# Kernel tuning notes

Hardware: AMD Instinct MI355X
Metric: run time of the kernel (lower is better)

The kernel has to match this reference:

```python
import jax, jax.numpy as jnp
import numpy as np

B, T_FRAMES, C, WS = 8, 8, 32, 128
N = 1024            # sample_size^2 points per frame
HW = WS * WS        # 16384 grid cells
BT = B * T_FRAMES


def setup_inputs() -> dict:
    key = jax.random.key(0)
    k1, k2, k3 = jax.random.split(key, 3)
    rng = np.random.default_rng(0)
    # per-frame grid-cell id for each of N points
    pose = rng.integers(0, HW, size=(BT, N))
    sorted_indices = np.argsort(pose, axis=1).astype(np.int32)
    sorted_pose = np.take_along_axis(pose, sorted_indices, axis=1)
    seq_unique_list = np.zeros((BT, N), dtype=np.int32)
    seq_unique_counts = np.zeros((BT, N), dtype=np.int32)
    for i in range(BT):
        u, c = np.unique(sorted_pose[i], return_counts=True)
        seq_unique_list[i, : len(u)] = u
        seq_unique_counts[i, : len(u)] = c
    return {
        "w_part": jax.random.normal(k1, (BT, N, C), dtype=jnp.float32),
        "sorted_indices": jnp.asarray(sorted_indices),
        "seq_unique_list": jnp.asarray(seq_unique_list),
        "seq_unique_counts": jnp.asarray(seq_unique_counts),
        "past_w": jax.random.normal(k2, (B, C, WS, WS), dtype=jnp.float32),
        "past_w_num_mask": jax.random.uniform(k3, (B, 1, WS, WS), dtype=jnp.float32) * 4.0,
        "T": T_FRAMES,
    }


def reference(w_part, sorted_indices, seq_unique_list, seq_unique_counts, past_w, past_w_num_mask, T):
    bt, n, c = w_part.shape
    b = bt // T
    ws = past_w.shape[2]
    hw = ws * ws
    # F.normalize(dim=-1), eps=1e-12
    wp = w_part / jnp.maximum(jnp.linalg.norm(w_part, axis=-1, keepdims=True), 1e-12)
    # gather: reorder points so same-cell points are contiguous
    gathered = jnp.take_along_axis(wp, sorted_indices[..., None].astype(jnp.int32), axis=1)  # (bt, n, c)
    counts = seq_unique_counts  # (bt, n) padded with zeros
    # segment id of each point from cumulative counts (points are sorted by cell)
    cum = jnp.cumsum(counts, axis=1)
    pt = jnp.arange(n)
    seg = jax.vmap(lambda cu: jnp.searchsorted(cu, pt, side='right'))(cum)  # (bt, n)
    sums = jax.vmap(lambda g, s: jax.ops.segment_sum(g, s, num_segments=n))(gathered, seg)  # (bt, n, c)
    means = sums / jnp.maximum(counts, 1)[..., None].astype(wp.dtype)
    # scatter means into dense grid; padded (count==0) slots routed out-of-bounds and dropped
    idx = jnp.where(counts > 0, seq_unique_list, hw)
    scat = jax.vmap(lambda m, i: jnp.zeros((hw, c), wp.dtype).at[i].set(m, mode='drop'))(means, idx)  # (bt, hw, c)
    mask = jax.vmap(lambda ct, i: jnp.zeros((hw,), wp.dtype).at[i].set(ct.astype(wp.dtype), mode='drop'))(counts, idx)
    new_w = scat.reshape(b, T, hw, c).mean(axis=1)                 # (b, hw, c)
    new_w = new_w.transpose(0, 2, 1).reshape(b, c, ws, ws)          # (b, c, ws, ws)
    w_num_mask = mask.reshape(b, T, hw).sum(axis=1).reshape(b, 1, ws, ws)
    # merge with past map; denominator is detached in the original
    new_w_num_mask = jax.lax.stop_gradient(w_num_mask) + jax.lax.stop_gradient(past_w_num_mask)
    new_w_num_mask = jnp.where(new_w_num_mask == 0, 1.0, new_w_num_mask)
    w = (new_w * w_num_mask + past_w * past_w_num_mask) / new_w_num_mask
    return w, new_w_num_mask
```

## Files before the change

kernel.cpp:

```cpp
#include <hip/hip_runtime.h>
#include <climits>

#define BATCH   8
#define TFRAMES 8
#define BT      (BATCH * TFRAMES)
#define NPTS    1024
#define NCH     32
#define WS      128
#define HW      (WS * WS)
#define CELLS   128
#define CHUNKS  (HW / CELLS)
#define CPAD    33
#define TPB     512

__global__ __launch_bounds__(256) void scan_kernel(
    const int* __restrict__ uniq_cnt,
    const int* __restrict__ uniq_list,
    int4*      __restrict__ entries,
    int*       __restrict__ ranges)
{
    __shared__ int s_key[NPTS];
    __shared__ int s_wsum[4];

    const int tid  = threadIdx.x;
    const int bt   = blockIdx.x;
    const int wave = tid >> 6;
    const int lane = tid & 63;

    const int4 c4 = reinterpret_cast<const int4*>(uniq_cnt + bt * NPTS)[tid];
    const int4 l4 = reinterpret_cast<const int4*>(uniq_list + bt * NPTS)[tid];
    s_key[tid * 4 + 0] = (c4.x > 0) ? l4.x : INT_MAX;
    s_key[tid * 4 + 1] = (c4.y > 0) ? l4.y : INT_MAX;
    s_key[tid * 4 + 2] = (c4.z > 0) ? l4.z : INT_MAX;
    s_key[tid * 4 + 3] = (c4.w > 0) ? l4.w : INT_MAX;

    const int lsum = c4.x + c4.y + c4.z + c4.w;

    int inc = lsum;
#pragma unroll
    for (int d = 1; d < 64; d <<= 1) {
        const int v = __shfl_up(inc, d);
        if (lane >= d) inc += v;
    }
    if (lane == 63) s_wsum[wave] = inc;
    __syncthreads();

    int woff = 0;
#pragma unroll
    for (int w = 0; w < 4; ++w)
        if (w < wave) woff += s_wsum[w];

    int st = woff + inc - lsum;
    int4* ep = entries + (size_t)bt * NPTS + tid * 4;
    ep[0] = make_int4(l4.x, c4.x, st, 0);             st += c4.x;
    ep[1] = make_int4(l4.y, c4.y, st, 0);             st += c4.y;
    ep[2] = make_int4(l4.z, c4.z, st, 0);             st += c4.z;
    ep[3] = make_int4(l4.w, c4.w, st, 0);

    if (tid <= CHUNKS) {
        const int X = tid * CELLS;
        int lo = 0, hi = NPTS;
        while (lo < hi) {
            const int mid = (lo + hi) >> 1;
            if (s_key[mid] < X) lo = mid + 1; else hi = mid;
        }
        ranges[bt * (CHUNKS + 1) + tid] = lo;
    }
}

__global__ __launch_bounds__(TPB) void tile_kernel(
    const float* __restrict__ w_part,
    const int*   __restrict__ sorted_idx,
    const int4*  __restrict__ entries,
    const int*   __restrict__ ranges,
    const float* __restrict__ past_w,
    const float* __restrict__ past_mask,
    float*       __restrict__ out_w,
    float*       __restrict__ out_mask)
{
    __shared__ float s_acc[CELLS][CPAD];
    __shared__ float s_mask[CELLS];

    const int tid      = threadIdx.x;
    const int b        = blockIdx.x / CHUNKS;
    const int chunk    = blockIdx.x % CHUNKS;
    const int cellBase = chunk * CELLS;

    const int cellq = tid & 31;
    const int cgrp  = tid >> 5;
    const int c0    = cgrp * 2;
    const int gc    = cellBase + cellq * 4;
    const size_t mbase = (size_t)b * HW + gc;
    const float4 pm4 = *reinterpret_cast<const float4*>(past_mask + mbase);
    const size_t a0 = ((size_t)b * NCH + c0) * HW + gc;
    const float4 pw0 = *reinterpret_cast<const float4*>(past_w + a0);
    const float4 pw1 = *reinterpret_cast<const float4*>(past_w + a0 + HW);

    float* flat = &s_acc[0][0];
    for (int i = tid; i < CELLS * CPAD; i += TPB) flat[i] = 0.0f;
    if (tid < CELLS) s_mask[tid] = 0.0f;
    __syncthreads();

    const int wave  = tid >> 6;
    const int lane  = tid & 63;
    const int slot  = lane >> 3;
    const int lane8 = lane & 7;

    const int bt = b * TFRAMES + wave;
    const int lo = ranges[bt * (CHUNKS + 1) + chunk];
    const int hi = ranges[bt * (CHUNKS + 1) + chunk + 1];
    const int4* __restrict__ ent = entries + (size_t)bt * NPTS;
    const int*  __restrict__ si  = sorted_idx + bt * NPTS;
    const float* __restrict__ wp = w_part + (size_t)bt * NPTS * NCH;

    for (int e0 = lo; e0 < hi; e0 += 8) {
        const int e = e0 + slot;
        if (e < hi) {
            const int4 meta = ent[e];
            const int cell  = meta.x;
            const int cnt   = meta.y;
            const int start = meta.z;
            float4 lacc = make_float4(0.f, 0.f, 0.f, 0.f);
            for (int p = start; p < start + cnt; ++p) {
                const int j = si[p];
                const float4 v = *reinterpret_cast<const float4*>(
                    wp + (size_t)j * NCH + lane8 * 4);
                float ss = v.x * v.x + v.y * v.y + v.z * v.z + v.w * v.w;
                ss += __shfl_xor(ss, 1);
                ss += __shfl_xor(ss, 2);
                ss += __shfl_xor(ss, 4);
                const float scale = 1.0f / fmaxf(sqrtf(ss), 1e-12f);
                lacc.x += v.x * scale;
                lacc.y += v.y * scale;
                lacc.z += v.z * scale;
                lacc.w += v.w * scale;
            }
            const float invc = 1.0f / (float)cnt;
            const int cl = cell - cellBase;
            float* ap = &s_acc[cl][lane8 * 4];
            atomicAdd(ap + 0, lacc.x * invc);
            atomicAdd(ap + 1, lacc.y * invc);
            atomicAdd(ap + 2, lacc.z * invc);
            atomicAdd(ap + 3, lacc.w * invc);
            if (lane8 == 0) atomicAdd(&s_mask[cl], (float)cnt);
        }
    }
    __syncthreads();

    const float invT = 1.0f / (float)TFRAMES;
    float m[4], pm[4], r[4], dn[4];
    pm[0] = pm4.x; pm[1] = pm4.y; pm[2] = pm4.z; pm[3] = pm4.w;
#pragma unroll
    for (int i = 0; i < 4; ++i) {
        m[i] = s_mask[cellq * 4 + i];
        const float nwm = m[i] + pm[i];
        dn[i] = (nwm == 0.0f) ? 1.0f : nwm;
        r[i] = 1.0f / dn[i];
    }
    if (cgrp == 0) {
        *reinterpret_cast<float4*>(out_mask + mbase) =
            make_float4(dn[0], dn[1], dn[2], dn[3]);
    }

    float4 o0, o1;
    o0.x = (s_acc[cellq * 4 + 0][c0] * invT * m[0] + pw0.x * pm[0]) * r[0];
    o0.y = (s_acc[cellq * 4 + 1][c0] * invT * m[1] + pw0.y * pm[1]) * r[1];
    o0.z = (s_acc[cellq * 4 + 2][c0] * invT * m[2] + pw0.z * pm[2]) * r[2];
    o0.w = (s_acc[cellq * 4 + 3][c0] * invT * m[3] + pw0.w * pm[3]) * r[3];
    o1.x = (s_acc[cellq * 4 + 0][c0 + 1] * invT * m[0] + pw1.x * pm[0]) * r[0];
    o1.y = (s_acc[cellq * 4 + 1][c0 + 1] * invT * m[1] + pw1.y * pm[1]) * r[1];
    o1.z = (s_acc[cellq * 4 + 2][c0 + 1] * invT * m[2] + pw1.z * pm[2]) * r[2];
    o1.w = (s_acc[cellq * 4 + 3][c0 + 1] * invT * m[3] + pw1.w * pm[3]) * r[3];
    *reinterpret_cast<float4*>(out_w + a0)      = o0;
    *reinterpret_cast<float4*>(out_w + a0 + HW) = o1;
}

extern "C" void kernel_launch(void* const* d_in, const int* in_sizes, int n_in,
                              void* d_out, int out_size, void* d_ws, size_t ws_size,
                              hipStream_t stream) {
    (void)in_sizes; (void)n_in; (void)out_size; (void)ws_size;

    const float* w_part     = (const float*)d_in[0];
    const int*   sorted_idx = (const int*)d_in[1];
    const int*   uniq_list  = (const int*)d_in[2];
    const int*   uniq_cnt   = (const int*)d_in[3];
    const float* past_w     = (const float*)d_in[4];
    const float* past_mask  = (const float*)d_in[5];

    float* out      = (float*)d_out;
    float* out_w    = out;
    float* out_mask = out + (size_t)BATCH * NCH * HW;

    int4* entries = (int4*)d_ws;
    int*  ranges  = (int*)(entries + (size_t)BT * NPTS);

    scan_kernel<<<BT, 256, 0, stream>>>(uniq_cnt, uniq_list, entries, ranges);

    tile_kernel<<<BATCH * CHUNKS, TPB, 0, stream>>>(
        w_part, sorted_idx, entries, ranges,
        past_w, past_mask, out_w, out_mask);
}
```

Before: 30.03 us.

## Fuse scan into tile kernel by recomputing per-frame prefix sums per block

Removes the separate scan kernel and its workspace round-trip. Each tile block's wave now reloads the full count and list arrays for its frame, computes the prefix sums with shuffles, and compacts the entries that fall in its cell chunk into shared memory. The block-to-(batch, chunk) mapping is also changed so that blocks for the same chunk of different batches sit next to each other. The cost is redundant work: every one of the 1024 blocks rescans 1024 entries per frame, which replaces one launch and the entries/ranges traffic.

```diff
diff --git a/kernel.cpp b/kernel.cpp
--- a/kernel.cpp
+++ b/kernel.cpp
@@ -12,67 +12,13 @@
 #define CHUNKS  (HW / CELLS)
 #define CPAD    33
 #define TPB     512
-
-__global__ __launch_bounds__(256) void scan_kernel(
-    const int* __restrict__ uniq_cnt,
-    const int* __restrict__ uniq_list,
-    int4*      __restrict__ entries,
-    int*       __restrict__ ranges)
-{
-    __shared__ int s_key[NPTS];
-    __shared__ int s_wsum[4];
-
-    const int tid  = threadIdx.x;
-    const int bt   = blockIdx.x;
-    const int wave = tid >> 6;
-    const int lane = tid & 63;
-
-    const int4 c4 = reinterpret_cast<const int4*>(uniq_cnt + bt * NPTS)[tid];
-    const int4 l4 = reinterpret_cast<const int4*>(uniq_list + bt * NPTS)[tid];
-    s_key[tid * 4 + 0] = (c4.x > 0) ? l4.x : INT_MAX;
-    s_key[tid * 4 + 1] = (c4.y > 0) ? l4.y : INT_MAX;
-    s_key[tid * 4 + 2] = (c4.z > 0) ? l4.z : INT_MAX;
-    s_key[tid * 4 + 3] = (c4.w > 0) ? l4.w : INT_MAX;
-
-    const int lsum = c4.x + c4.y + c4.z + c4.w;
-
-    int inc = lsum;
-#pragma unroll
-    for (int d = 1; d < 64; d <<= 1) {
-        const int v = __shfl_up(inc, d);
-        if (lane >= d) inc += v;
-    }
-    if (lane == 63) s_wsum[wave] = inc;
-    __syncthreads();
-
-    int woff = 0;
-#pragma unroll
-    for (int w = 0; w < 4; ++w)
-        if (w < wave) woff += s_wsum[w];
-
-    int st = woff + inc - lsum;
-    int4* ep = entries + (size_t)bt * NPTS + tid * 4;
-    ep[0] = make_int4(l4.x, c4.x, st, 0);             st += c4.x;
-    ep[1] = make_int4(l4.y, c4.y, st, 0);             st += c4.y;
-    ep[2] = make_int4(l4.z, c4.z, st, 0);             st += c4.z;
-    ep[3] = make_int4(l4.w, c4.w, st, 0);
-
-    if (tid <= CHUNKS) {
-        const int X = tid * CELLS;
-        int lo = 0, hi = NPTS;
-        while (lo < hi) {
-            const int mid = (lo + hi) >> 1;
-            if (s_key[mid] < X) lo = mid + 1; else hi = mid;
-        }
-        ranges[bt * (CHUNKS + 1) + tid] = lo;
-    }
-}
-
-__global__ __launch_bounds__(TPB) void tile_kernel(
+#define MAXE    CELLS
+
+__global__ __launch_bounds__(TPB) void fused_kernel(
     const float* __restrict__ w_part,
     const int*   __restrict__ sorted_idx,
-    const int4*  __restrict__ entries,
-    const int*   __restrict__ ranges,
+    const int*   __restrict__ uniq_list,
+    const int*   __restrict__ uniq_cnt,
     const float* __restrict__ past_w,
     const float* __restrict__ past_mask,
     float*       __restrict__ out_w,
@@ -80,16 +26,19 @@
 {
     __shared__ float s_acc[CELLS][CPAD];
     __shared__ float s_mask[CELLS];
-
-    const int tid      = threadIdx.x;
-    const int b        = blockIdx.x / CHUNKS;
-    const int chunk    = blockIdx.x % CHUNKS;
-    const int cellBase = chunk * CELLS;
+    __shared__ int   s_cell[TFRAMES][MAXE];
+    __shared__ int   s_cntl[TFRAMES][MAXE];
+    __shared__ int   s_sta [TFRAMES][MAXE];
+
+    const int tid   = threadIdx.x;
+    const int b     = blockIdx.x & (BATCH - 1);
+    const int chunk = blockIdx.x >> 3;
+    const int cb    = chunk * CELLS;
 
     const int cellq = tid & 31;
     const int cgrp  = tid >> 5;
     const int c0    = cgrp * 2;
-    const int gc    = cellBase + cellq * 4;
+    const int gc    = cb + cellq * 4;
     const size_t mbase = (size_t)b * HW + gc;
     const float4 pm4 = *reinterpret_cast<const float4*>(past_mask + mbase);
     const size_t a0 = ((size_t)b * NCH + c0) * HW + gc;
@@ -99,27 +48,89 @@
     float* flat = &s_acc[0][0];
     for (int i = tid; i < CELLS * CPAD; i += TPB) flat[i] = 0.0f;
     if (tid < CELLS) s_mask[tid] = 0.0f;
+
+    const int wave = tid >> 6;
+    const int lane = tid & 63;
+    const int bt   = b * TFRAMES + wave;
+
+    const int4* cb4 = reinterpret_cast<const int4*>(uniq_cnt  + bt * NPTS);
+    const int4* lb4 = reinterpret_cast<const int4*>(uniq_list + bt * NPTS);
+
+    int4 c4s[4], l4s[4];
+#pragma unroll
+    for (int k = 0; k < 4; ++k) {
+        c4s[k] = cb4[lane * 4 + k];
+        l4s[k] = lb4[lane * 4 + k];
+    }
+
+    int lane_total = 0;
+    int first_e    = INT_MAX;
+    int n_in       = 0;
+#pragma unroll
+    for (int k = 0; k < 4; ++k) {
+        const int cc[4] = {c4s[k].x, c4s[k].y, c4s[k].z, c4s[k].w};
+        const int ll[4] = {l4s[k].x, l4s[k].y, l4s[k].z, l4s[k].w};
+#pragma unroll
+        for (int j = 0; j < 4; ++j) {
+            const bool inr = (cc[j] > 0) && (ll[j] >= cb) && (ll[j] < cb + CELLS);
+            if (inr) {
+                ++n_in;
+                const int e = lane * 16 + k * 4 + j;
+                if (e < first_e) first_e = e;
+            }
+            lane_total += cc[j];
+        }
+    }
+
+    int inc = lane_total;
+#pragma unroll
+    for (int d = 1; d < 64; d <<= 1) {
+        const int v = __shfl_up(inc, d);
+        if (lane >= d) inc += v;
+    }
+    const int lane_base = inc - lane_total;
+
+    int lo = first_e;
+    int ne = n_in;
+#pragma unroll
+    for (int d = 1; d < 64; d <<= 1) {
+        lo = min(lo, __shfl_xor(lo, d));
+        ne += __shfl_xor(ne, d);
+    }
+
+    int running = lane_base;
+#pragma unroll
+    for (int k = 0; k < 4; ++k) {
+        const int cc[4] = {c4s[k].x, c4s[k].y, c4s[k].z, c4s[k].w};
+        const int ll[4] = {l4s[k].x, l4s[k].y, l4s[k].z, l4s[k].w};
+#pragma unroll
+        for (int j = 0; j < 4; ++j) {
+            const bool inr = (cc[j] > 0) && (ll[j] >= cb) && (ll[j] < cb + CELLS);
+            if (inr) {
+                const int e   = lane * 16 + k * 4 + j;
+                const int idx = e - lo;
+                s_cell[wave][idx] = ll[j];
+                s_cntl[wave][idx] = cc[j];
+                s_sta [wave][idx] = running;
+            }
+            running += cc[j];
+        }
+    }
+
     __syncthreads();
 
-    const int wave  = tid >> 6;
-    const int lane  = tid & 63;
     const int slot  = lane >> 3;
     const int lane8 = lane & 7;
 
-    const int bt = b * TFRAMES + wave;
-    const int lo = ranges[bt * (CHUNKS + 1) + chunk];
-    const int hi = ranges[bt * (CHUNKS + 1) + chunk + 1];
-    const int4* __restrict__ ent = entries + (size_t)bt * NPTS;
-    const int*  __restrict__ si  = sorted_idx + bt * NPTS;
+    const int*   __restrict__ si = sorted_idx + bt * NPTS;
     const float* __restrict__ wp = w_part + (size_t)bt * NPTS * NCH;
 
-    for (int e0 = lo; e0 < hi; e0 += 8) {
+    for (int e0 = 0; e0 < ne; e0 += 8) {
         const int e = e0 + slot;
-        if (e < hi) {
-            const int4 meta = ent[e];
-            const int cell  = meta.x;
-            const int cnt   = meta.y;
-            const int start = meta.z;
+        if (e < ne) {
+            const int cell  = s_cell[wave][e];
+            const int cnt   = s_cntl[wave][e];
+            const int start = s_sta [wave][e];
             float4 lacc = make_float4(0.f, 0.f, 0.f, 0.f);
             for (int p = start; p < start + cnt; ++p) {
                 const int j = si[p];
@@ -136,7 +147,7 @@
                 lacc.w += v.w * scale;
             }
             const float invc = 1.0f / (float)cnt;
-            const int cl = cell - cellBase;
+            const int cl = cell - cb;
             float* ap = &s_acc[cl][lane8 * 4];
             atomicAdd(ap + 0, lacc.x * invc);
             atomicAdd(ap + 1, lacc.y * invc);
@@ -178,7 +189,7 @@
 extern "C" void kernel_launch(void* const* d_in, const int* in_sizes, int n_in,
                               void* d_out, int out_size, void* d_ws, size_t ws_size,
                               hipStream_t stream) {
-    (void)in_sizes; (void)n_in; (void)out_size; (void)ws_size;
+    (void)in_sizes; (void)n_in; (void)out_size; (void)d_ws; (void)ws_size;
 
     const float* w_part     = (const float*)d_in[0];
     const int*   sorted_idx = (const int*)d_in[1];
@@ -191,12 +202,7 @@
     float* out_w    = out;
     float* out_mask = out + (size_t)BATCH * NCH * HW;
 
-    int4* entries = (int4*)d_ws;
-    int*  ranges  = (int*)(entries + (size_t)BT * NPTS);
-
-    scan_kernel<<<BT, 256, 0, stream>>>(uniq_cnt, uniq_list, entries, ranges);
-
-    tile_kernel<<<BATCH * CHUNKS, TPB, 0, stream>>>(
-        w_part, sorted_idx, entries, ranges,
+    fused_kernel<<<BATCH * CHUNKS, TPB, 0, stream>>>(
+        w_part, sorted_idx, uniq_list, uniq_cnt,
         past_w, past_mask, out_w, out_mask);
 }
```

Result: slower. 31.72 us (+5.6%).
